# Kernel tuning notes

Measured on AMD Instinct MI355X. Metric: run time of the kernel, lower is better.

Reference implementation:

```python
import jax, jax.numpy as jnp
import numpy as np
from math import factorial, sqrt

L = 8
RCUT = 5.0
PI = 3.14159  # literal used in the torch module's Ylm normalization
N_POINTS = 4194304


def powcmplx(zr, zi, n):
    # Faithful port, including the n>2 recurrence that uses the *updated*
    # real part when forming the imaginary part (as in the source).
    if n == 0:
        return jnp.ones_like(zr), jnp.zeros_like(zr)
    if n == 1:
        return zr, zi
    if n == 2:
        return zr * zr - zi * zi, 2.0 * zr * zi
    r, im = zr, zi
    for _ in range(2, n + 1):
        r = zr * r - zi * im
        im = zr * im + zi * r  # uses updated r, matching the source exactly
    return r, im


def _forward(pos):
    norms = jnp.sqrt(jnp.sum(pos * pos, axis=1))
    valid = norms > 0
    mask = valid.astype(pos.dtype)
    safe = jnp.where(valid, norms, 1.0)
    # cosine_cutoff uses the true pi (acos trick in the source)
    cut = 0.5 * (jnp.cos(norms * (jnp.pi / RCUT)) + 1.0)
    cut = jnp.where(norms > RCUT, 0.0, cut) * mask  # mask replaces boolean row-select
    xp_r = -0.5 * pos[:, 0]
    xp_i = -0.5 * pos[:, 1]
    xm_r = 0.5 * pos[:, 0]
    xm_i = -0.5 * pos[:, 1]
    x0 = pos[:, 2]
    n_out = (L + 1) ** 2
    vals = [jnp.zeros((), pos.dtype)] * n_out
    i = 0
    for l in range(L + 1):
        w_l = cut / safe ** l * sqrt((2 * l + 1) / 4 / PI)  # per-point weight for this l
        for M in range(-l, 1):
            m = abs(M)
            sr = jnp.zeros_like(x0)
            si = jnp.zeros_like(x0)
            for p in range(l + 1):
                q = p - m
                s = l - p - q
                if q >= 0 and s >= 0:
                    z1r, z1i = powcmplx(xp_r, xp_i, p)
                    z2r, z2i = powcmplx(xm_r, xm_i, q)
                    zr = z1r ** 2 - z2i ** 2      # faithful to source (squared terms)
                    zi = z1r * z2i + z1i * z2r
                    c = 1.0 / (factorial(p) * factorial(q) * factorial(s))
                    sr = sr + zr * x0 * c          # source multiplies by x0 (x0**s is unused there)
                    si = si + zi * x0 * c
            f = sqrt(factorial(l + m) * factorial(l - m))
            w = f * w_l
            clm_r = jnp.sum(sr * w)
            clm_i = jnp.sum(si * w)
            if m == 0:
                vals[i] = clm_r
            else:
                fac = sqrt(2.0) * (-1) ** m
                vals[i] = fac * clm_i
                vals[i + 2 * m] = fac * clm_r
            i += 1
        i += l
    return jnp.stack(vals).reshape(-1, 1)


def setup_inputs() -> dict:
    key = jax.random.key(0)
    pos = jax.random.normal(key, (N_POINTS, 3), dtype=jnp.float32) * 2.0
    return {"pos": pos}


def reference(pos):
    return _forward(pos)
```

## Files before the change

kernel.cpp:

```cpp
#include <hip/hip_runtime.h>
#include <math.h>


#define NL 8
#define NACC 45
#define NBLK 1024

__device__ __forceinline__ float waveReduce(float v) {
    v += __shfl_down(v, 32);
    v += __shfl_down(v, 16);
    v += __shfl_down(v, 8);
    v += __shfl_down(v, 4);
    v += __shfl_down(v, 2);
    v += __shfl_down(v, 1);
    return v;
}

__global__ __launch_bounds__(256, 1)
void sht_main(const float* __restrict__ pos, float* __restrict__ ws, int n) {
    const float FACT[9] = {1.f, 1.f, 2.f, 6.f, 24.f, 120.f, 720.f, 5040.f, 40320.f};

    float accr[NACC];
    float acci[NACC];
#pragma unroll
    for (int i = 0; i < NACC; ++i) { accr[i] = 0.f; acci[i] = 0.f; }

    const int tid = blockIdx.x * blockDim.x + threadIdx.x;
    const int stride = gridDim.x * blockDim.x;

    for (int i = tid; i < n; i += stride) {
        const float x = pos[3 * i + 0];
        const float y = pos[3 * i + 1];
        const float z = pos[3 * i + 2];

        const float r2 = x * x + y * y + z * z;
        const bool valid = r2 > 0.0f;
        const float inv0 = __builtin_amdgcn_rsqf(r2);
        const float norm = r2 * inv0;
        float cut = 0.5f * (__cosf(norm * 0.6283185307179586f) + 1.0f);
        cut = (r2 > 25.0f) ? 0.0f : cut;
        cut = valid ? cut : 0.0f;
        const float inv = valid ? inv0 : 1.0f;
        const float x0c = z * cut;

        const float xpr = -0.5f * x, xpi = -0.5f * y;
        const float xmr = 0.5f * x, xmi = -0.5f * y;

        float a[9], b[9], c2[9], d[9];
        a[0] = 1.f; b[0] = 0.f; a[1] = xpr; b[1] = xpi;
        c2[0] = 1.f; d[0] = 0.f; c2[1] = xmr; d[1] = xmi;
        a[2] = xpr * xpr - xpi * xpi; b[2] = 2.f * xpr * xpi;
        c2[2] = xmr * xmr - xmi * xmi; d[2] = 2.f * xmr * xmi;
        {
            float br = a[2];
            float bi = xpr * xpi + xpi * br;
#pragma unroll
            for (int k = 3; k <= NL; ++k) {
                const float nr = xpr * br - xpi * bi;
                const float ni = xpr * bi + xpi * nr;
                br = nr; bi = ni;
                a[k] = br; b[k] = bi;
            }
        }
        {
            float br = c2[2];
            float bi = xmr * xmi + xmi * br;
#pragma unroll
            for (int k = 3; k <= NL; ++k) {
                const float nr = xmr * br - xmi * bi;
                const float ni = xmr * bi + xmi * nr;
                br = nr; bi = ni;
                c2[k] = br; d[k] = bi;
            }
        }

        float sqa[9];
#pragma unroll
        for (int p = 0; p <= NL; ++p) sqa[p] = a[p] * a[p];

        float h[9];
        h[0] = x0c;
#pragma unroll
        for (int l = 1; l <= NL; ++l) h[l] = h[l - 1] * inv;

        float Yr[9][9], Yi[9][9];
#pragma unroll
        for (int p = 0; p <= NL; ++p) {
#pragma unroll
            for (int q = 0; q <= NL; ++q) {
                if (q <= p && p + q <= NL) {
                    const float cpq = 1.0f / (FACT[p] * FACT[q]);
                    Yr[p][q] = fmaf(-d[q], d[q], sqa[p]) * cpq;
                    if (q != p)
                        Yi[p][q] = fmaf(a[p], d[q], b[p] * c2[q]) * cpq;
                }
            }
        }

#pragma unroll
        for (int l = 0; l <= NL; ++l) {
#pragma unroll
            for (int m = 0; m <= NL; ++m) {
                if (m <= l) {
                    float sr = 0.f, si = 0.f;
#pragma unroll
                    for (int p = 0; p <= NL; ++p) {
                        if (p >= m && 2 * p - m <= l) {
                            const int q = p - m;
                            const int s = l - 2 * p + m;
                            const float is = 1.0f / FACT[s];
                            sr = fmaf(Yr[p][q], is, sr);
                            if (m > 0) si = fmaf(Yi[p][q], is, si);
                        }
                    }
                    const int ai = l * (l + 1) / 2 + m;
                    accr[ai] = fmaf(sr, h[l], accr[ai]);
                    if (m > 0) acci[ai] = fmaf(si, h[l], acci[ai]);
                }
            }
        }
    }

    __shared__ float red[81][5];
    const int lane = threadIdx.x & 63;
    const int wave = threadIdx.x >> 6;

#pragma unroll
    for (int m = 0; m <= NL; ++m) {
#pragma unroll
        for (int l = m; l <= NL; ++l) {
            const int ai = l * (l + 1) / 2 + m;
            float vr = waveReduce(accr[ai]);
            if (lane == 0) red[l * l + l + m][wave] = vr;
            if (m > 0) {
                float vi = waveReduce(acci[ai]);
                if (lane == 0) red[l * l + l - m][wave] = vi;
            }
        }
    }
    __syncthreads();

    if ((int)threadIdx.x < 81) {
        float s = 0.f;
#pragma unroll
        for (int w = 0; w < 4; ++w) s += red[threadIdx.x][w];
        ws[(size_t)threadIdx.x * NBLK + blockIdx.x] = s;
    }
}

__device__ double dfact(int nn) {
    double r = 1.0;
    for (int i = 2; i <= nn; ++i) r *= (double)i;
    return r;
}

__global__ __launch_bounds__(256)
void sht_finalize(const float* __restrict__ ws, float* __restrict__ out) {
    const int j = blockIdx.x;
    const int t = threadIdx.x;
    float s = 0.f;
#pragma unroll
    for (int k = 0; k < NBLK / 256; ++k)
        s += ws[(size_t)j * NBLK + k * 256 + t];
    s = waveReduce(s);

    __shared__ float red[4];
    const int lane = t & 63, wave = t >> 6;
    if (lane == 0) red[wave] = s;
    __syncthreads();
    if (t == 0) {
        float tot = red[0] + red[1] + red[2] + red[3];
        int l = 0;
        while ((l + 1) * (l + 1) <= j) ++l;
        const int M = j - l * l - l;
        const int m = (M < 0) ? -M : M;
        double sc = sqrt(dfact(l + m) * dfact(l - m)) *
                    sqrt((double)(2 * l + 1) / (4.0 * 3.14159));
        if (m > 0) sc *= sqrt(2.0) * ((m & 1) ? -1.0 : 1.0);
        out[j] = (float)((double)tot * sc);
    }
}

extern "C" void kernel_launch(void* const* d_in, const int* in_sizes, int n_in,
                              void* d_out, int out_size, void* d_ws, size_t ws_size,
                              hipStream_t stream) {
    const float* pos = (const float*)d_in[0];
    const int npts = in_sizes[0] / 3;
    float* ws = (float*)d_ws;
    float* out = (float*)d_out;

    sht_main<<<NBLK, 256, 0, stream>>>(pos, ws, npts);
    sht_finalize<<<81, 256, 0, stream>>>(ws, out);
}
```

Baseline: 153.3 us.

## Pack real/imag accumulation into float2 FMAs and load four points per thread

Rewrites the per-point body to hold the plus and minus complex powers and the real/imag partial sums as 2-wide float vectors. This lets the compiler emit packed FMA instructions and halves the scalar FMA count. Each thread now loads four points through three aligned float4 loads instead of strided scalar loads, and launch bounds allow two blocks per CU. Risks include higher register pressure from the packed accumulators and the per-m Y arrays, possible spills at the tighter occupancy bound, and extra wasted work on the m=0 imaginary lanes.

```diff
diff --git a/kernel.cpp b/kernel.cpp
--- a/kernel.cpp
+++ b/kernel.cpp
@@ -1,10 +1,17 @@
 #include <hip/hip_runtime.h>
 #include <math.h>
 
+
+typedef float f32x2 __attribute__((ext_vector_type(2)));
 
 #define NL 8
 #define NACC 45
 #define NBLK 1024
+#define NTHR 256
+
+__device__ __forceinline__ f32x2 pkfma(f32x2 a, f32x2 b, f32x2 c) {
+    return __builtin_elementwise_fma(a, b, c);
+}
 
 __device__ __forceinline__ float waveReduce(float v) {
     v += __shfl_down(v, 32);
@@ -16,109 +23,123 @@
     return v;
 }
 
-__global__ __launch_bounds__(256, 1)
+__device__ __forceinline__ void point_body(float x, float y, float z,
+                                           f32x2* __restrict__ accp) {
+    const float FACT[9] = {1.f, 1.f, 2.f, 6.f, 24.f, 120.f, 720.f, 5040.f, 40320.f};
+
+    const float r2 = x * x + y * y + z * z;
+    const bool valid = r2 > 0.0f;
+    const float inv0 = __builtin_amdgcn_rsqf(r2);
+    const float norm = r2 * inv0;
+    float cut = 0.5f * (__cosf(norm * 0.6283185307179586f) + 1.0f);
+    cut = (r2 > 25.0f) ? 0.0f : cut;
+    cut = valid ? cut : 0.0f;
+    const float inv = valid ? inv0 : 1.0f;
+    const float x0c = z * cut;
+
+    const f32x2 w  = { -0.5f * x,  0.5f * x };
+    const f32x2 wi = { -0.5f * y, -0.5f * y };
+
+    f32x2 zr[9], zi[9];
+    zr[0] = f32x2{1.f, 1.f}; zi[0] = f32x2{0.f, 0.f};
+    zr[1] = w;               zi[1] = wi;
+    zr[2] = w * w - wi * wi;
+    zi[2] = (w + w) * wi;
+    {
+        f32x2 cr = zr[2];
+        f32x2 ci = w * wi + wi * cr;
+#pragma unroll
+        for (int k = 3; k <= NL; ++k) {
+            const f32x2 nr = w * cr - wi * ci;
+            const f32x2 ni = w * ci + wi * nr;
+            cr = nr; ci = ni;
+            zr[k] = nr; zi[k] = ni;
+        }
+    }
+
+    float aa[9], bb[9], cc[9], dd[9], sqa[9];
+#pragma unroll
+    for (int p = 0; p <= NL; ++p) {
+        aa[p] = zr[p].x;
+        cc[p] = zr[p].y;
+        bb[p] = zi[p].x;
+        dd[p] = zi[p].y;
+        sqa[p] = aa[p] * aa[p];
+    }
+
+    float h[9];
+    h[0] = x0c;
+#pragma unroll
+    for (int l = 1; l <= NL; ++l) h[l] = h[l - 1] * inv;
+
+#pragma unroll
+    for (int m = 0; m <= NL; ++m) {
+        f32x2 Y[9];
+#pragma unroll
+        for (int p = 0; p <= NL; ++p) {
+            if (p >= m && 2 * p - m <= NL) {
+                const int q = p - m;
+                const float cpq = 1.0f / (FACT[p] * FACT[q]);
+                const float bc = bb[p] * cc[q];
+                const f32x2 A = { -dd[q], aa[p] };
+                const f32x2 B = {  dd[q], dd[q] };
+                const f32x2 C = { sqa[p], bc };
+                const f32x2 Yv = pkfma(A, B, C);
+                Y[p] = Yv * f32x2{cpq, cpq};
+            }
+        }
+#pragma unroll
+        for (int l = m; l <= NL; ++l) {
+            f32x2 s = {0.f, 0.f};
+#pragma unroll
+            for (int p = 0; p <= NL; ++p) {
+                if (p >= m && 2 * p - m <= l) {
+                    const int sidx = l - 2 * p + m;
+                    const float is = 1.0f / FACT[sidx];
+                    s = pkfma(Y[p], f32x2{is, is}, s);
+                }
+            }
+            const int ai = l * (l + 1) / 2 + m;
+            accp[ai] = pkfma(s, f32x2{h[l], h[l]}, accp[ai]);
+        }
+    }
+}
+
+__global__ __launch_bounds__(256, 2)
 void sht_main(const float* __restrict__ pos, float* __restrict__ ws, int n) {
-    const float FACT[9] = {1.f, 1.f, 2.f, 6.f, 24.f, 120.f, 720.f, 5040.f, 40320.f};
-
-    float accr[NACC];
-    float acci[NACC];
-#pragma unroll
-    for (int i = 0; i < NACC; ++i) { accr[i] = 0.f; acci[i] = 0.f; }
-
-    const int tid = blockIdx.x * blockDim.x + threadIdx.x;
-    const int stride = gridDim.x * blockDim.x;
-
-    for (int i = tid; i < n; i += stride) {
-        const float x = pos[3 * i + 0];
-        const float y = pos[3 * i + 1];
-        const float z = pos[3 * i + 2];
-
-        const float r2 = x * x + y * y + z * z;
-        const bool valid = r2 > 0.0f;
-        const float inv0 = __builtin_amdgcn_rsqf(r2);
-        const float norm = r2 * inv0;
-        float cut = 0.5f * (__cosf(norm * 0.6283185307179586f) + 1.0f);
-        cut = (r2 > 25.0f) ? 0.0f : cut;
-        cut = valid ? cut : 0.0f;
-        const float inv = valid ? inv0 : 1.0f;
-        const float x0c = z * cut;
-
-        const float xpr = -0.5f * x, xpi = -0.5f * y;
-        const float xmr = 0.5f * x, xmi = -0.5f * y;
-
-        float a[9], b[9], c2[9], d[9];
-        a[0] = 1.f; b[0] = 0.f; a[1] = xpr; b[1] = xpi;
-        c2[0] = 1.f; d[0] = 0.f; c2[1] = xmr; d[1] = xmi;
-        a[2] = xpr * xpr - xpi * xpi; b[2] = 2.f * xpr * xpi;
-        c2[2] = xmr * xmr - xmi * xmi; d[2] = 2.f * xmr * xmi;
-        {
-            float br = a[2];
-            float bi = xpr * xpi + xpi * br;
-#pragma unroll
-            for (int k = 3; k <= NL; ++k) {
-                const float nr = xpr * br - xpi * bi;
-                const float ni = xpr * bi + xpi * nr;
-                br = nr; bi = ni;
-                a[k] = br; b[k] = bi;
-            }
-        }
-        {
-            float br = c2[2];
-            float bi = xmr * xmi + xmi * br;
-#pragma unroll
-            for (int k = 3; k <= NL; ++k) {
-                const float nr = xmr * br - xmi * bi;
-                const float ni = xmr * bi + xmi * nr;
-                br = nr; bi = ni;
-                c2[k] = br; d[k] = bi;
-            }
-        }
-
-        float sqa[9];
-#pragma unroll
-        for (int p = 0; p <= NL; ++p) sqa[p] = a[p] * a[p];
-
-        float h[9];
-        h[0] = x0c;
-#pragma unroll
-        for (int l = 1; l <= NL; ++l) h[l] = h[l - 1] * inv;
-
-        float Yr[9][9], Yi[9][9];
-#pragma unroll
-        for (int p = 0; p <= NL; ++p) {
-#pragma unroll
-            for (int q = 0; q <= NL; ++q) {
-                if (q <= p && p + q <= NL) {
-                    const float cpq = 1.0f / (FACT[p] * FACT[q]);
-                    Yr[p][q] = fmaf(-d[q], d[q], sqa[p]) * cpq;
-                    if (q != p)
-                        Yi[p][q] = fmaf(a[p], d[q], b[p] * c2[q]) * cpq;
-                }
-            }
-        }
-
-#pragma unroll
-        for (int l = 0; l <= NL; ++l) {
-#pragma unroll
-            for (int m = 0; m <= NL; ++m) {
-                if (m <= l) {
-                    float sr = 0.f, si = 0.f;
-#pragma unroll
-                    for (int p = 0; p <= NL; ++p) {
-                        if (p >= m && 2 * p - m <= l) {
-                            const int q = p - m;
-                            const int s = l - 2 * p + m;
-                            const float is = 1.0f / FACT[s];
-                            sr = fmaf(Yr[p][q], is, sr);
-                            if (m > 0) si = fmaf(Yi[p][q], is, si);
-                        }
-                    }
-                    const int ai = l * (l + 1) / 2 + m;
-                    accr[ai] = fmaf(sr, h[l], accr[ai]);
-                    if (m > 0) acci[ai] = fmaf(si, h[l], acci[ai]);
-                }
-            }
-        }
+    f32x2 accp[NACC];
+#pragma unroll
+    for (int i = 0; i < NACC; ++i) accp[i] = f32x2{0.f, 0.f};
+
+    const int t = blockIdx.x * NTHR + threadIdx.x;
+    const int nthreads = NBLK * NTHR;
+    const int nchunks = (n / 4 + nthreads - 1) / nthreads;
+
+    for (int c = 0; c < nchunks; ++c) {
+        const int idx = (c * nthreads + t) * 4;
+        float xs[4], ys[4], zs[4];
+        if (idx + 4 <= n) {
+            const float4* p4 = reinterpret_cast<const float4*>(pos + (size_t)3 * idx);
+            const float4 q0 = p4[0];
+            const float4 q1 = p4[1];
+            const float4 q2 = p4[2];
+            xs[0] = q0.x; ys[0] = q0.y; zs[0] = q0.z;
+            xs[1] = q0.w; ys[1] = q1.x; zs[1] = q1.y;
+            xs[2] = q1.z; ys[2] = q1.w; zs[2] = q2.x;
+            xs[3] = q2.y; ys[3] = q2.z; zs[3] = q2.w;
+        } else {
+#pragma unroll
+            for (int k = 0; k < 4; ++k) {
+                const int i = idx + k;
+                const bool ok = i < n;
+                xs[k] = ok ? pos[3 * i + 0] : 0.f;
+                ys[k] = ok ? pos[3 * i + 1] : 0.f;
+                zs[k] = ok ? pos[3 * i + 2] : 0.f;
+            }
+        }
+#pragma unroll
+        for (int k = 0; k < 4; ++k)
+            point_body(xs[k], ys[k], zs[k], accp);
     }
 
     __shared__ float red[81][5];
@@ -130,10 +151,10 @@
 #pragma unroll
         for (int l = m; l <= NL; ++l) {
             const int ai = l * (l + 1) / 2 + m;
-            float vr = waveReduce(accr[ai]);
+            float vr = waveReduce(accp[ai].x);
             if (lane == 0) red[l * l + l + m][wave] = vr;
             if (m > 0) {
-                float vi = waveReduce(acci[ai]);
+                float vi = waveReduce(accp[ai].y);
                 if (lane == 0) red[l * l + l - m][wave] = vi;
             }
         }
@@ -189,6 +210,6 @@
     float* ws = (float*)d_ws;
     float* out = (float*)d_out;
 
-    sht_main<<<NBLK, 256, 0, stream>>>(pos, ws, npts);
+    sht_main<<<NBLK, NTHR, 0, stream>>>(pos, ws, npts);
     sht_finalize<<<81, 256, 0, stream>>>(ws, out);
 }
```

Result: faster. 139.9 us (-8.7%).
